# Performance work log

Hardware: AMD Instinct MI355X
Metric: run time of the kernel (lower is better)

The kernel has to match this reference:

```python
import jax, jax.numpy as jnp
import numpy as np

B, M, P = 128, 35, 224  # batch, num Zernike modes, pupil_size
SIGN_PENALTY = 10.0
RECON_WEIGHT = 0.4
DEFOCUS_RAD = 1.0
EPS = 1e-8


def setup_inputs() -> dict:
    key = jax.random.key(0)
    k1, k2, k3, k4 = jax.random.split(key, 4)
    pred = jax.random.normal(k1, (B, M), dtype=jnp.float32)
    target = jax.random.normal(k2, (B, M), dtype=jnp.float32)
    input_psfs = jax.random.uniform(k3, (B, 2, P, P), dtype=jnp.float32)
    zernike_basis = jax.random.normal(k4, (M, P, P), dtype=jnp.float32)
    pupil_mask = jnp.ones((P, P), dtype=jnp.float32)
    return {
        "pred": pred,
        "target": target,
        "input_psfs": input_psfs,
        "zernike_basis": zernike_basis,
        "pupil_mask": pupil_mask,
    }


def _psf_from_phase(phase, pupil_mask):
    # phase: [B,P,P] real; pupil: masked complex field
    pupil = pupil_mask[None, :, :] * jnp.exp(1j * phase)
    field = jnp.fft.fftshift(jnp.fft.fft2(pupil), axes=(-2, -1))
    psf = field.real ** 2 + field.imag ** 2  # |FFT|^2
    psf = psf / (psf.sum(axis=(-2, -1), keepdims=True) + EPS)
    return psf


def reference(pred, target, input_psfs, zernike_basis, pupil_mask):
    # --- sign-weighted MSE on Zernike coefficients ---
    base = (pred - target) ** 2
    sign_match = jnp.sign(pred) * jnp.sign(target)
    weight = jnp.where(sign_match < 0, SIGN_PENALTY, 1.0)
    z_loss = jnp.mean(base * weight)

    # --- batched differentiable PSF reconstruction loss ---
    phase = jnp.einsum('bm,mhw->bhw', pred, zernike_basis)
    phase = phase * pupil_mask[None, :, :]

    sim_if = _psf_from_phase(phase, pupil_mask)  # in-focus

    lin = jnp.linspace(-1.0, 1.0, P, dtype=jnp.float32)
    y, x = jnp.meshgrid(lin, lin, indexing='ij')
    r2 = x ** 2 + y ** 2
    defocus_phase = DEFOCUS_RAD * (2.0 * r2 - 1.0)  # [P,P]
    sim_podf = _psf_from_phase(phase + defocus_phase[None, :, :], pupil_mask)

    # per-sample F.mse_loss then mean over batch == mean over the batched arrays
    recon_loss = (jnp.mean((sim_if - input_psfs[:, 0]) ** 2)
                  + jnp.mean((sim_podf - input_psfs[:, 1]) ** 2))

    return z_loss + RECON_WEIGHT * recon_loss
```

## Files before the change

### kernel.cpp

```cpp
#include <hip/hip_runtime.h>
#include <math.h>

#define BB 128
#define MM 35
#define PSZ 224
#define PP (PSZ*PSZ)
#define SIGN_PENALTY 10.0f
#define RECON_WEIGHT 0.4f
#define DEFOCUS_RAD 1.0f
#define EPS_F 1e-8f
#define INV2PI 0.15915494309189535f


#define WS_PHASE_OFF    2048
#define WS_T_OFF        (WS_PHASE_OFF + BB*PP)
#define N_PARTIALS      (14*BB*2)
#define S1 233
#define S2 20

static constexpr float W16R[16] = {
    1.0f, 0.9238795325f, 0.7071067812f, 0.3826834324f, 0.0f,
    -0.3826834324f, -0.7071067812f, -0.9238795325f, -1.0f,
    -0.9238795325f, -0.7071067812f, -0.3826834324f, 0.0f,
    0.3826834324f, 0.7071067812f, 0.9238795325f};
static constexpr float W16I[16] = {
    0.0f, -0.3826834324f, -0.7071067812f, -0.9238795325f, -1.0f,
    -0.9238795325f, -0.7071067812f, -0.3826834324f, 0.0f,
    0.3826834324f, 0.7071067812f, 0.9238795325f, 1.0f,
    0.9238795325f, 0.7071067812f, 0.3826834324f};
static constexpr float W7R[7] = {
    1.0f, 0.6234898019f, -0.2225209340f, -0.9009688679f,
    -0.9009688679f, -0.2225209340f, 0.6234898019f};
static constexpr float W7I[7] = {
    0.0f, -0.7818314825f, -0.9749279122f, -0.4338837391f,
    0.4338837391f, 0.9749279122f, 0.7818314825f};
static constexpr float W14R[7] = {
    1.0f, 0.9009688679f, 0.6234898019f, 0.2225209340f, -0.2225209340f,
    -0.6234898019f, -0.9009688679f};
static constexpr float W14I[7] = {
    0.0f, -0.4338837391f, -0.7818314825f, -0.9749279122f, -0.9749279122f,
    -0.7818314825f, -0.4338837391f};

__device__ __forceinline__ float lincoord(int i) {
    return -1.0f + 2.0f * (float)i / (float)(PSZ - 1);
}
__device__ __forceinline__ void fast_sincos(float x, float* s, float* c) {
    float rv = x * INV2PI;
    rv -= floorf(rv);
    *s = __builtin_amdgcn_sinf(rv);
    *c = __builtin_amdgcn_cosf(rv);
}
__device__ __forceinline__ float2 wexp_neg(float frac) {
    float rv = -frac;
    rv -= floorf(rv);
    return make_float2(__builtin_amdgcn_cosf(rv), __builtin_amdgcn_sinf(rv));
}
__device__ __forceinline__ unsigned pack_bf2(float a, float b) {
    unsigned r;
    asm("v_cvt_pk_bf16_f32 %0, %1, %2" : "=v"(r) : "v"(a), "v"(b));
    return r;
}
__device__ __forceinline__ float2 unpack_bf2(unsigned v) {
    return make_float2(__uint_as_float(v << 16), __uint_as_float(v & 0xffff0000u));
}
__device__ __forceinline__ float2 cmul(float2 a, float2 b) {
    return make_float2(fmaf(a.x, b.x, -a.y * b.y), fmaf(a.x, b.y, a.y * b.x));
}
__device__ __forceinline__ float2 cmulc(float2 a, float wr, float wi) {
    return make_float2(fmaf(a.x, wr, -a.y * wi), fmaf(a.x, wi, a.y * wr));
}
__device__ __forceinline__ float2 cadd(float2 a, float2 b) {
    return make_float2(a.x + b.x, a.y + b.y);
}
__device__ __forceinline__ float2 csub(float2 a, float2 b) {
    return make_float2(a.x - b.x, a.y - b.y);
}
__device__ __forceinline__ void cfma(float& acc, float c, float v) {
    if (c == 0.f) return;
    if (c == 1.f)  { acc += v; return; }
    if (c == -1.f) { acc -= v; return; }
    acc = fmaf(c, v, acc);
}

__device__ __forceinline__ void dft8_sym(const float2* u, float2* X) {
    float2 a1 = cadd(u[1], u[7]), b1 = csub(u[1], u[7]);
    float2 a2 = cadd(u[2], u[6]), b2 = csub(u[2], u[6]);
    float2 a3 = cadd(u[3], u[5]), b3 = csub(u[3], u[5]);
    float2 s04 = cadd(u[0], u[4]), d04 = csub(u[0], u[4]);
    X[0] = cadd(cadd(s04, a1), cadd(a2, a3));
    X[4] = cadd(csub(s04, a1), csub(a2, a3));
    {
        float2 p = csub(s04, a2);
        float2 q = csub(b1, b3);
        X[2] = make_float2(p.x + q.y, p.y - q.x);
        X[6] = make_float2(p.x - q.y, p.y + q.x);
    }
#pragma unroll
    for (int m = 1; m <= 3; m += 2) {
        float Px = d04.x, Py = d04.y, Qx = 0.f, Qy = 0.f;
#pragma unroll
        for (int n = 1; n <= 3; n++) {
            const float cR = W16R[(2 * n * m) & 15], cI = W16I[(2 * n * m) & 15];
            const float2 a = (n == 1) ? a1 : (n == 2) ? a2 : a3;
            const float2 b = (n == 1) ? b1 : (n == 2) ? b2 : b3;
            cfma(Px, cR, a.x); cfma(Py, cR, a.y);
            cfma(Qx, cI, b.x); cfma(Qy, cI, b.y);
        }
        X[m]     = make_float2(Px - Qy, Py + Qx);
        X[8 - m] = make_float2(Px + Qy, Py - Qx);
    }
}

__device__ __forceinline__ void dft7_sym(const float2* x, float2* X) {
    float2 a1 = cadd(x[1], x[6]), b1 = csub(x[1], x[6]);
    float2 a2 = cadd(x[2], x[5]), b2 = csub(x[2], x[5]);
    float2 a3 = cadd(x[3], x[4]), b3 = csub(x[3], x[4]);
    X[0] = cadd(cadd(x[0], a1), cadd(a2, a3));
#pragma unroll
    for (int k = 1; k <= 3; k++) {
        float Px = x[0].x, Py = x[0].y, Qx = 0.f, Qy = 0.f;
#pragma unroll
        for (int n = 1; n <= 3; n++) {
            const float cR = W7R[(n * k) % 7], cI = W7I[(n * k) % 7];
            const float2 a = (n == 1) ? a1 : (n == 2) ? a2 : a3;
            const float2 b = (n == 1) ? b1 : (n == 2) ? b2 : b3;
            cfma(Px, cR, a.x); cfma(Py, cR, a.y);
            cfma(Qx, cI, b.x); cfma(Qy, cI, b.y);
        }
        X[k]     = make_float2(Px - Qy, Py + Qx);
        X[7 - k] = make_float2(Px + Qy, Py - Qx);
    }
}

__device__ __forceinline__ void inner16_core(const float2* xin,
                                             unsigned* __restrict__ xbuf,
                                             int base, int mul, int n1) {
    float2 u[8], v[8];
#pragma unroll
    for (int n = 0; n < 8; n++) {
        u[n] = cadd(xin[n], xin[n + 8]);
        float2 w = csub(xin[n], xin[n + 8]);
        v[n] = (n == 0) ? w : cmulc(w, W16R[n], W16I[n]);
    }
    float2 u1w = wexp_neg((float)n1 * (1.0f / 224.0f));
    float2 u2w = wexp_neg((float)n1 * (1.0f / 112.0f));
    {
        float2 Xe[8];
        dft8_sym(u, Xe);
        float2 cur = make_float2(1.f, 0.f);
#pragma unroll
        for (int m = 0; m < 8; m++) {
            float2 z = (m == 0) ? Xe[0] : cmul(Xe[m], cur);
            xbuf[base + (14 * (2 * m)) * mul] = pack_bf2(z.x, z.y);
            cur = cmul(cur, u2w);
        }
    }
    {
        float2 Xo[8];
        dft8_sym(v, Xo);
        float2 cur = u1w;
#pragma unroll
        for (int m = 0; m < 8; m++) {
            float2 z = cmul(Xo[m], cur);
            xbuf[base + (14 * (2 * m + 1)) * mul] = pack_bf2(z.x, z.y);
            cur = cmul(cur, u2w);
        }
    }
}

__global__ __launch_bounds__(256) void k_phase(const float* __restrict__ pred,
                                               const float* __restrict__ target,
                                               const float* __restrict__ zern,
                                               const float* __restrict__ mask,
                                               unsigned* __restrict__ field,
                                               float* __restrict__ ws) {
    __shared__ __align__(16) float pl[32 * 36];
    __shared__ float red[256];
    int t = threadIdx.x;
    if (blockIdx.x == 196) {
        int y = blockIdx.y;
        float s = 0.f;
        if (y == 0) {
            for (int i = t; i < BB * MM; i += 256) {
                float p = pred[i], tg = target[i];
                float dd = p - tg;
                float w = (p * tg < 0.f) ? SIGN_PENALTY : 1.f;
                s = fmaf(dd * dd, w, s);
            }
        } else {
            const int F4 = PP / 4;
            int st = (y - 1) * 4182;
            int en = (y == 3) ? F4 : st + 4182;
            const float4* m4 = (const float4*)mask;
            for (int i = st + t; i < en; i += 256) {
                float4 v = m4[i];
                s = fmaf(v.x, v.x, s); s = fmaf(v.y, v.y, s);
                s = fmaf(v.z, v.z, s); s = fmaf(v.w, v.w, s);
            }
        }
        red[t] = s;
        __syncthreads();
        for (int st = 128; st > 0; st >>= 1) {
            if (t < st) red[t] += red[t + st];
            __syncthreads();
        }
        if (t == 0) {
            if (y == 0) ws[1] = red[0] / (float)(BB * MM);
            else        ws[1 + y] = red[0];
        }
        return;
    }
    int bg = blockIdx.y;
    for (int i = t; i < 32 * MM; i += 256) {
        int j = i / MM, m = i - (i / MM) * MM;
        pl[j * 36 + m] = pred[(bg * 32 + j) * MM + m];
    }
    if (t < 32) pl[t * 36 + 35] = 0.f;
    __syncthreads();
    int pix = blockIdx.x * 256 + t;
    float acc[32];
#pragma unroll
    for (int j = 0; j < 32; j++) acc[j] = 0.f;
    const float4* pl4 = (const float4*)pl;
    for (int mb = 0; mb < 32; mb += 4) {
        float z0 = zern[(size_t)(mb + 0) * PP + pix];
        float z1 = zern[(size_t)(mb + 1) * PP + pix];
        float z2 = zern[(size_t)(mb + 2) * PP + pix];
        float z3 = zern[(size_t)(mb + 3) * PP + pix];
#pragma unroll
        for (int j = 0; j < 32; j++) {
            float4 p4 = pl4[j * 9 + (mb >> 2)];
            acc[j] = fmaf(p4.x, z0, acc[j]);
            acc[j] = fmaf(p4.y, z1, acc[j]);
            acc[j] = fmaf(p4.z, z2, acc[j]);
            acc[j] = fmaf(p4.w, z3, acc[j]);
        }
    }
    {
        float z0 = zern[(size_t)32 * PP + pix];
        float z1 = zern[(size_t)33 * PP + pix];
        float z2 = zern[(size_t)34 * PP + pix];
#pragma unroll
        for (int j = 0; j < 32; j++) {
            float4 p4 = pl4[j * 9 + 8];
            acc[j] = fmaf(p4.x, z0, acc[j]);
            acc[j] = fmaf(p4.y, z1, acc[j]);
            acc[j] = fmaf(p4.z, z2, acc[j]);
        }
    }
    float mk = mask[pix];
#pragma unroll
    for (int j = 0; j < 32; j++) {
        float ph = acc[j] * mk;
        float sn, cs;
        fast_sincos(ph, &sn, &cs);
        field[(size_t)(bg * 32 + j) * PP + pix] = pack_bf2(mk * cs, mk * sn);
    }
}

__global__ __launch_bounds__(256, 4) void k_stage1(const unsigned* __restrict__ field,
                                                   unsigned* __restrict__ T) {
    __shared__ unsigned xs0[16 * S1];
    __shared__ unsigned xs1[16 * S1];
    int h0 = blockIdx.x * 16;
    int b = blockIdx.y;
    int t = threadIdx.x;

    if (t < 224) {
        int r = t / 14, n1 = t - (t / 14) * 14;
        const unsigned* fr = field + (size_t)b * PP + (size_t)(h0 + r) * PSZ;
        float vy = lincoord(h0 + r);
        float vy2m1 = DEFOCUS_RAD * (2.f * vy * vy - 1.f);
        float2 x0[16];
        unsigned x1p[16];
#pragma unroll
        for (int n = 0; n < 16; n++) {
            int col = n1 + 14 * n;
            float2 f = unpack_bf2(fr[col]);
            float vx = lincoord(col);
            float df = fmaf(2.f * DEFOCUS_RAD, vx * vx, vy2m1);
            float sd, cd;
            fast_sincos(df, &sd, &cd);
            x0[n] = f;
            x1p[n] = pack_bf2(fmaf(f.x, cd, -f.y * sd), fmaf(f.y, cd, f.x * sd));
        }
        inner16_core(x0, xs0, r * S1 + n1, 1, n1);
        float2 x1[16];
#pragma unroll
        for (int n = 0; n < 16; n++) x1[n] = unpack_bf2(x1p[n]);
        inner16_core(x1, xs1, r * S1 + n1, 1, n1);
    }
    __syncthreads();

    {
        int r = t >> 4, k2 = t & 15;
#pragma unroll
        for (int dd = 0; dd < 2; dd++) {
            const unsigned* xr = (dd ? xs1 : xs0) + r * S1 + k2 * 14;
            int img = dd * BB + b;
            unsigned* Tt = T + (((size_t)img * 14) * PSZ + (h0 + r)) * 16 + k2;
            float2 e[7], E[7], O[7];
#pragma unroll
            for (int n = 0; n < 7; n++) e[n] = unpack_bf2(xr[2 * n]);
            dft7_sym(e, E);
#pragma unroll
            for (int n = 0; n < 7; n++) e[n] = unpack_bf2(xr[2 * n + 1]);
            dft7_sym(e, O);
#pragma unroll
            for (int k1 = 0; k1 < 7; k1++) {
                float2 op = (k1 == 0) ? O[0] : cmulc(O[k1], W14R[k1], W14I[k1]);
                float2 s = cadd(E[k1], op), q = csub(E[k1], op);
                Tt[(size_t)k1 * (PSZ * 16)]       = pack_bf2(s.x, s.y);
                Tt[(size_t)(k1 + 7) * (PSZ * 16)] = pack_bf2(q.x, q.y);
            }
        }
    }
}

__global__ __launch_bounds__(256, 5) void k_stage2(const unsigned* __restrict__ T,
                                                   const float* __restrict__ psfs,
                                                   const float* __restrict__ ws,
                                                   float* __restrict__ partials) {
    __shared__ unsigned xs[224 * S2];
    __shared__ float red[4];
    int tile = blockIdx.x, b = blockIdx.y, d = blockIdx.z;
    int img = d * BB + b;
    int t = threadIdx.x;
    int k2o = t >> 4, c = t & 15;
    bool act = t < 224;

    const unsigned* Tb = T + ((size_t)img * 14 + tile) * (PSZ * 16);
    const float* inp = psfs + ((size_t)b * 2 + d) * PP;
    int scol = 16 * ((tile + 7) % 14) + c;

    unsigned xr[16];
    if (act) {
#pragma unroll
        for (int n = 0; n < 16; n++) xr[n] = Tb[224 * n + t];
    }
    float pf[14];
#pragma unroll
    for (int j = 0; j < 7; j++) {
        pf[j]     = inp[(size_t)(112 + 16 * j + k2o) * PSZ + scol];
        pf[j + 7] = inp[(size_t)(16 * j + k2o) * PSZ + scol];
    }

    if (act) {
        float2 x[16];
#pragma unroll
        for (int n = 0; n < 16; n++) x[n] = unpack_bf2(xr[n]);
        inner16_core(x, xs, (t >> 4) * S2 + (t & 15), S2, t >> 4);
    }
    __syncthreads();

    float m2 = ws[2] + ws[3] + ws[4];
    float inv_denom = 1.f / (m2 * (float)PP + EPS_F);

    float lsum = 0.f;
    {
        float2 e[7], E[7], O[7];
#pragma unroll
        for (int n = 0; n < 7; n++) e[n] = unpack_bf2(xs[(k2o * 14 + 2 * n) * S2 + c]);
        dft7_sym(e, E);
#pragma unroll
        for (int n = 0; n < 7; n++) e[n] = unpack_bf2(xs[(k2o * 14 + 2 * n + 1) * S2 + c]);
        dft7_sym(e, O);
#pragma unroll
        for (int k1 = 0; k1 < 7; k1++) {
            float2 op = (k1 == 0) ? O[0] : cmulc(O[k1], W14R[k1], W14I[k1]);
            float2 s = cadd(E[k1], op), q = csub(E[k1], op);
            float ds = fmaf(s.x, s.x, s.y * s.y) * inv_denom - pf[k1];
            float dq = fmaf(q.x, q.x, q.y * q.y) * inv_denom - pf[k1 + 7];
            lsum = fmaf(ds, ds, lsum);
            lsum = fmaf(dq, dq, lsum);
        }
    }
#pragma unroll
    for (int off = 32; off > 0; off >>= 1)
        lsum += __shfl_down(lsum, off, 64);
    if ((t & 63) == 0) red[t >> 6] = lsum;
    __syncthreads();
    if (t == 0)
        partials[(blockIdx.z * BB + blockIdx.y) * 14 + blockIdx.x] =
            red[0] + red[1] + red[2] + red[3];
}

__global__ void k_final(const float* __restrict__ ws,
                        const float* __restrict__ partials,
                        float* __restrict__ out) {
    __shared__ float red[256];
    float s = 0.f;
    for (int i = threadIdx.x; i < N_PARTIALS; i += 256) s += partials[i];
    red[threadIdx.x] = s;
    __syncthreads();
    for (int st = 128; st > 0; st >>= 1) {
        if (threadIdx.x < st) red[threadIdx.x] += red[threadIdx.x + st];
        __syncthreads();
    }
    if (threadIdx.x == 0) {
        float recon = red[0] / (float)((size_t)BB * PP);
        out[0] = ws[1] + RECON_WEIGHT * recon;
    }
}

extern "C" void kernel_launch(void* const* d_in, const int* in_sizes, int n_in,
                              void* d_out, int out_size, void* d_ws, size_t ws_size,
                              hipStream_t stream) {
    const float* pred   = (const float*)d_in[0];
    const float* target = (const float*)d_in[1];
    const float* psfs   = (const float*)d_in[2];
    const float* zern   = (const float*)d_in[3];
    const float* mask   = (const float*)d_in[4];

    float*    ws       = (float*)d_ws;
    unsigned* field    = (unsigned*)(ws + WS_PHASE_OFF);
    float*    partials = ws + WS_PHASE_OFF;
    unsigned* T        = (unsigned*)(ws + WS_T_OFF);
    float*    out      = (float*)d_out;

    k_phase<<<dim3(197, 4), 256, 0, stream>>>(pred, target, zern, mask, field, ws);
    k_stage1<<<dim3(14, BB), 256, 0, stream>>>(field, T);
    k_stage2<<<dim3(14, BB, 2), 256, 0, stream>>>(T, psfs, ws, partials);
    k_final<<<1, 256, 0, stream>>>(ws, partials, out);
}
```

Before: 154.6 us.

## Split stage1 per focus plane and use separable defocus phasor tables

Stage1 now launches one block per (row tile, focus plane, batch) instead of processing both in-focus and defocused fields in one block, which halves shared memory per block and raises the occupancy hint. The per-element defocus sincos is replaced by a separable product of precomputed column and row phasor tables written by k_phase, so each element costs one complex multiply. In exchange, each field row is read twice from global memory (once per plane), and the table values are stored in fp32 instead of the bf16 round-trip of the rotated field.

```diff
diff --git a/kernel.cpp b/kernel.cpp
--- a/kernel.cpp
+++ b/kernel.cpp
@@ -181,6 +181,16 @@
         int y = blockIdx.y;
         float s = 0.f;
         if (y == 0) {
+            if (t < 224) {
+                float v = lincoord(t);
+                float fc = fmaf(2.f * DEFOCUS_RAD, v * v, -DEFOCUS_RAD);
+                float fr = 2.f * DEFOCUS_RAD * v * v;
+                float sn, cs;
+                fast_sincos(fc, &sn, &cs);
+                ((float2*)(ws + 16))[t] = make_float2(cs, sn);
+                fast_sincos(fr, &sn, &cs);
+                ((float2*)(ws + 512))[t] = make_float2(cs, sn);
+            }
             for (int i = t; i < BB * MM; i += 256) {
                 float p = pred[i], tg = target[i];
                 float dd = p - tg;
@@ -258,61 +268,55 @@
     }
 }
 
-__global__ __launch_bounds__(256, 4) void k_stage1(const unsigned* __restrict__ field,
+__global__ __launch_bounds__(256, 5) void k_stage1(const unsigned* __restrict__ field,
+                                                   const float* __restrict__ ws,
                                                    unsigned* __restrict__ T) {
-    __shared__ unsigned xs0[16 * S1];
-    __shared__ unsigned xs1[16 * S1];
+    __shared__ unsigned xs[16 * S1];
     int h0 = blockIdx.x * 16;
-    int b = blockIdx.y;
+    int d = blockIdx.y, b = blockIdx.z;
     int t = threadIdx.x;
 
     if (t < 224) {
         int r = t / 14, n1 = t - (t / 14) * 14;
-        const unsigned* fr = field + (size_t)b * PP + (size_t)(h0 + r) * PSZ;
-        float vy = lincoord(h0 + r);
-        float vy2m1 = DEFOCUS_RAD * (2.f * vy * vy - 1.f);
+        const unsigned* frow = field + (size_t)b * PP + (size_t)(h0 + r) * PSZ;
         float2 x0[16];
-        unsigned x1p[16];
-#pragma unroll
-        for (int n = 0; n < 16; n++) {
-            int col = n1 + 14 * n;
-            float2 f = unpack_bf2(fr[col]);
-            float vx = lincoord(col);
-            float df = fmaf(2.f * DEFOCUS_RAD, vx * vx, vy2m1);
-            float sd, cd;
-            fast_sincos(df, &sd, &cd);
-            x0[n] = f;
-            x1p[n] = pack_bf2(fmaf(f.x, cd, -f.y * sd), fmaf(f.y, cd, f.x * sd));
-        }
-        inner16_core(x0, xs0, r * S1 + n1, 1, n1);
-        float2 x1[16];
-#pragma unroll
-        for (int n = 0; n < 16; n++) x1[n] = unpack_bf2(x1p[n]);
-        inner16_core(x1, xs1, r * S1 + n1, 1, n1);
+        if (d) {
+            const float2* ctab = (const float2*)(ws + 16);
+            const float2* rtab = (const float2*)(ws + 512);
+            float2 crow = rtab[h0 + r];
+#pragma unroll
+            for (int n = 0; n < 16; n++) {
+                int col = n1 + 14 * n;
+                float2 f = unpack_bf2(frow[col]);
+                float2 rot = cmul(crow, ctab[col]);
+                x0[n] = cmul(rot, f);
+            }
+        } else {
+#pragma unroll
+            for (int n = 0; n < 16; n++) x0[n] = unpack_bf2(frow[n1 + 14 * n]);
+        }
+        inner16_core(x0, xs, r * S1 + n1, 1, n1);
     }
     __syncthreads();
 
     {
         int r = t >> 4, k2 = t & 15;
-#pragma unroll
-        for (int dd = 0; dd < 2; dd++) {
-            const unsigned* xr = (dd ? xs1 : xs0) + r * S1 + k2 * 14;
-            int img = dd * BB + b;
-            unsigned* Tt = T + (((size_t)img * 14) * PSZ + (h0 + r)) * 16 + k2;
-            float2 e[7], E[7], O[7];
-#pragma unroll
-            for (int n = 0; n < 7; n++) e[n] = unpack_bf2(xr[2 * n]);
-            dft7_sym(e, E);
-#pragma unroll
-            for (int n = 0; n < 7; n++) e[n] = unpack_bf2(xr[2 * n + 1]);
-            dft7_sym(e, O);
-#pragma unroll
-            for (int k1 = 0; k1 < 7; k1++) {
-                float2 op = (k1 == 0) ? O[0] : cmulc(O[k1], W14R[k1], W14I[k1]);
-                float2 s = cadd(E[k1], op), q = csub(E[k1], op);
-                Tt[(size_t)k1 * (PSZ * 16)]       = pack_bf2(s.x, s.y);
-                Tt[(size_t)(k1 + 7) * (PSZ * 16)] = pack_bf2(q.x, q.y);
-            }
+        const unsigned* xr = xs + r * S1 + k2 * 14;
+        int img = d * BB + b;
+        unsigned* Tt = T + (((size_t)img * 14) * PSZ + (h0 + r)) * 16 + k2;
+        float2 e[7], E[7], O[7];
+#pragma unroll
+        for (int n = 0; n < 7; n++) e[n] = unpack_bf2(xr[2 * n]);
+        dft7_sym(e, E);
+#pragma unroll
+        for (int n = 0; n < 7; n++) e[n] = unpack_bf2(xr[2 * n + 1]);
+        dft7_sym(e, O);
+#pragma unroll
+        for (int k1 = 0; k1 < 7; k1++) {
+            float2 op = (k1 == 0) ? O[0] : cmulc(O[k1], W14R[k1], W14I[k1]);
+            float2 s = cadd(E[k1], op), q = csub(E[k1], op);
+            Tt[(size_t)k1 * (PSZ * 16)]       = pack_bf2(s.x, s.y);
+            Tt[(size_t)(k1 + 7) * (PSZ * 16)] = pack_bf2(q.x, q.y);
         }
     }
 }
@@ -419,7 +423,7 @@
     float*    out      = (float*)d_out;
 
     k_phase<<<dim3(197, 4), 256, 0, stream>>>(pred, target, zern, mask, field, ws);
-    k_stage1<<<dim3(14, BB), 256, 0, stream>>>(field, T);
+    k_stage1<<<dim3(14, 2, BB), 256, 0, stream>>>(field, ws, T);
     k_stage2<<<dim3(14, BB, 2), 256, 0, stream>>>(T, psfs, ws, partials);
     k_final<<<1, 256, 0, stream>>>(ws, partials, out);
 }
```

Result: no change. 153.0 us (-1.0%).
